# Kernel optimization log

Measured on AMD Instinct MI355X. Metric: run time of the kernel, lower is better.

The kernel has to match this reference:

```python
import jax, jax.numpy as jnp
import numpy as np

B, N, IN_DIM = 2, 512, 512
MEM, HID = 300, 64
NEG_SLOPE = 0.01


def setup_inputs() -> dict:
    key = jax.random.key(0)
    ks = jax.random.split(key, 10)
    feature = jax.random.normal(ks[0], (B, N, IN_DIM), dtype=jnp.float32)
    adj = jax.random.randint(ks[1], (B, N, N), 0, 2).astype(jnp.float32)
    s = 0.05
    # per-layer node projections W[l]
    w0 = jax.random.normal(ks[2], (IN_DIM, MEM), dtype=jnp.float32) * s
    b0 = jnp.zeros((MEM,), dtype=jnp.float32)
    w1 = jax.random.normal(ks[3], (MEM, MEM), dtype=jnp.float32) * s
    b1 = jnp.zeros((MEM,), dtype=jnp.float32)
    # shared attention MLP (afcs): Linear(2*MEM, HID) -> ReLU -> Linear(HID, 1)
    a1_w = jax.random.normal(ks[4], (2 * MEM, HID), dtype=jnp.float32) * s
    a1_b = jnp.zeros((HID,), dtype=jnp.float32)
    a2_w = jax.random.normal(ks[5], (HID, 1), dtype=jnp.float32) * s
    a2_b = jnp.zeros((1,), dtype=jnp.float32)
    return {"feature": feature, "adj": adj, "w0": w0, "b0": b0, "w1": w1,
            "b1": b1, "a1_w": a1_w, "a1_b": a1_b, "a2_w": a2_w, "a2_b": a2_b}


def _gat_layer(h_in, adj, w, b, a1_w, a1_b, a2_w, a2_b):
    h = h_in @ w + b                                   # (B,N,M)
    # cat([h_i, h_j]) @ a1_w split into the two halves (same math, no N^2*2M tensor)
    s_i = h @ a1_w[:MEM]                               # (B,N,H)
    s_j = h @ a1_w[MEM:]                               # (B,N,H)
    z = jax.nn.relu(s_i[:, :, None, :] + s_j[:, None, :, :] + a1_b)   # (B,N,N,H)
    e = (z @ a2_w)[..., 0] + a2_b[0]                   # (B,N,N)
    e = jax.nn.leaky_relu(e, negative_slope=NEG_SLOPE)
    b_, n_ = adj.shape[0], adj.shape[1]
    dmask = adj.reshape(b_, n_ * n_)
    logits = e.reshape(b_, n_ * n_) * dmask + (1.0 - dmask) * (-1e30)
    # NOTE: softmax over ALL N*N flattened edges (faithful to original dim=1)
    att = jax.nn.softmax(logits, axis=1).reshape(b_, n_, n_)
    return jnp.einsum('bij,bjd->bid', att, h)


def reference(feature, adj, w0, b0, w1, b1, a1_w, a1_b, a2_w, a2_b):
    f = _gat_layer(feature, adj, w0, b0, a1_w, a1_b, a2_w, a2_b)
    f = _gat_layer(f, adj, w1, b1, a1_w, a1_b, a2_w, a2_b)  # dropout = identity (eval)
    return f
```

## Files before the change

### kernel.cpp

```cpp
#include <hip/hip_runtime.h>

namespace {

constexpr int B_  = 2;
constexpr int N_  = 512;
constexpr int IN_ = 512;
constexpr int M_  = 300;
constexpr int H_  = 64;
constexpr float SLOPE_ = 0.01f;

constexpr long OFF_W0AI = 0;
constexpr long OFF_W0AJ = OFF_W0AI + 512L * 64;
constexpr long OFF_W1AI = OFF_W0AJ + 512L * 64;
constexpr long OFF_W1AJ = OFF_W1AI + 300L * 64;
constexpr long OFF_BSI0 = OFF_W1AJ + 300L * 64;
constexpr long OFF_BSJ0 = OFF_BSI0 + 64;
constexpr long OFF_BSI1 = OFF_BSJ0 + 64;
constexpr long OFF_BSJ1 = OFF_BSI1 + 64;
constexpr long OFF_H0   = OFF_BSJ1 + 64;
constexpr long OFF_SI0  = OFF_H0   + 1024L * 300;
constexpr long OFF_SJ0  = OFF_SI0  + 1024L * 64;
constexpr long OFF_F1   = OFF_SJ0  + 1024L * 64;
constexpr long OFF_H1   = OFF_F1   + 1024L * 300;
constexpr long OFF_SI1  = OFF_H1   + 1024L * 300;
constexpr long OFF_SJ1  = OFF_SI1  + 1024L * 64;
constexpr long OFF_ZP0  = OFF_SJ1  + 1024L * 64;
constexpr long OFF_ZP1  = OFF_ZP0  + 512;
constexpr long OFF_P0   = OFF_ZP1  + 512;
constexpr long OFF_P1   = OFF_P0   + 2L * 512 * 512;

struct Jobs {
    const float* A[8]; const float* W[8]; const float* bias[8]; const float* Zp[8];
    float* C[8];
    int K[8]; int lda[8]; int Cc[8]; int R[8];
    int off[8]; int njobs;
};

__global__ __launch_bounds__(256)
void gemm_multi(Jobs jb)
{
    __shared__ __align__(16) float As[32][38];
    __shared__ __align__(16) float Ws[32][64];

    const int bid = blockIdx.x;
    int j = jb.njobs - 1;
    while (j > 0 && bid < jb.off[j]) --j;
    const int local = bid - jb.off[j];

    const float* __restrict__ A = jb.A[j];
    const float* __restrict__ W = jb.W[j];
    const float* bias = jb.bias[j];
    const float* Zp   = jb.Zp[j];
    float* __restrict__ C = jb.C[j];
    const int K = jb.K[j], lda = jb.lda[j], Cc = jb.Cc[j], R = jb.R[j];

    const int tx   = (Cc + 63) >> 6;
    const int row0 = (local / tx) * 32;
    const int col0 = (local % tx) * 64;

    const int t   = threadIdx.x;
    const int ar  = t >> 3;
    const int ak  = (t & 7) * 4;
    const int arow = min(row0 + ar, R - 1);
    const int wk  = t >> 4;
    const int wc  = (t & 15) * 4;
    const int tm0 = (t >> 4) * 2;
    const int tn0 = (t & 15) * 4;

    auto loadA = [&](int k0) -> float4 {
        const int k = k0 + ak;
        if (k + 3 < K) return *(const float4*)(A + (long)arow * lda + k);
        float tv[4];
        #pragma unroll
        for (int u = 0; u < 4; ++u)
            tv[u] = (k + u < K) ? A[(long)arow * lda + k + u] : 0.0f;
        return make_float4(tv[0], tv[1], tv[2], tv[3]);
    };
    auto loadW = [&](int k0, int s) -> float4 {
        const int gk = k0 + wk + 16 * s;
        if (gk < K) {
            const int c = col0 + wc;
            if (c + 3 < Cc) return *(const float4*)(W + (long)gk * Cc + c);
            float tv[4];
            #pragma unroll
            for (int u = 0; u < 4; ++u)
                tv[u] = (c + u < Cc) ? W[(long)gk * Cc + c + u] : 0.0f;
            return make_float4(tv[0], tv[1], tv[2], tv[3]);
        }
        return make_float4(0.f, 0.f, 0.f, 0.f);
    };

    float acc[2][4] = {};
    float4 av  = loadA(0);
    float4 wv0 = loadW(0, 0);
    float4 wv1 = loadW(0, 1);

    for (int k0 = 0; k0 < K; k0 += 32) {
        As[ak + 0][ar] = av.x;
        As[ak + 1][ar] = av.y;
        As[ak + 2][ar] = av.z;
        As[ak + 3][ar] = av.w;
        *(float4*)&Ws[wk][wc]      = wv0;
        *(float4*)&Ws[wk + 16][wc] = wv1;
        __syncthreads();

        if (k0 + 32 < K) {
            av  = loadA(k0 + 32);
            wv0 = loadW(k0 + 32, 0);
            wv1 = loadW(k0 + 32, 1);
        }

        #pragma unroll
        for (int k = 0; k < 32; ++k) {
            const float a0 = As[k][tm0];
            const float a1 = As[k][tm0 + 1];
            const float4 w4 = *(const float4*)&Ws[k][tn0];
            acc[0][0] = fmaf(a0, w4.x, acc[0][0]);
            acc[0][1] = fmaf(a0, w4.y, acc[0][1]);
            acc[0][2] = fmaf(a0, w4.z, acc[0][2]);
            acc[0][3] = fmaf(a0, w4.w, acc[0][3]);
            acc[1][0] = fmaf(a1, w4.x, acc[1][0]);
            acc[1][1] = fmaf(a1, w4.y, acc[1][1]);
            acc[1][2] = fmaf(a1, w4.z, acc[1][2]);
            acc[1][3] = fmaf(a1, w4.w, acc[1][3]);
        }
        __syncthreads();
    }

    float scale = 1.0f;
    if (Zp != nullptr) {
        float s0 = 0.f, s1 = 0.f, s2 = 0.f, s3 = 0.f;
        for (int u = 0; u < 256; u += 4) {
            s0 += Zp[u]; s1 += Zp[u + 1]; s2 += Zp[u + 2]; s3 += Zp[u + 3];
        }
        scale = 1.0f / ((s0 + s1) + (s2 + s3));
    }
    const int cbase = col0 + tn0;
    float bv[4] = {0.f, 0.f, 0.f, 0.f};
    if (bias != nullptr) {
        #pragma unroll
        for (int u = 0; u < 4; ++u)
            if (cbase + u < Cc) bv[u] = bias[cbase + u];
    }
    #pragma unroll
    for (int i = 0; i < 2; ++i) {
        const int r = row0 + tm0 + i;
        if (r < R) {
            if (cbase + 3 < Cc) {
                float4 o;
                o.x = fmaf(acc[i][0], scale, bv[0]);
                o.y = fmaf(acc[i][1], scale, bv[1]);
                o.z = fmaf(acc[i][2], scale, bv[2]);
                o.w = fmaf(acc[i][3], scale, bv[3]);
                *(float4*)(C + (long)r * Cc + cbase) = o;
            } else {
                #pragma unroll
                for (int u = 0; u < 4; ++u)
                    if (cbase + u < Cc)
                        C[(long)r * Cc + cbase + u] = fmaf(acc[i][u], scale, bv[u]);
            }
        }
    }
}

__global__ __launch_bounds__(256)
void attn_p_kernel(const float* __restrict__ si, const float* __restrict__ sj,
                   const float* __restrict__ adj, const float* __restrict__ a2w,
                   const float* __restrict__ a2b, float* __restrict__ p,
                   float* __restrict__ Zpart)
{
    __shared__ __align__(16) float Si[32][68];
    __shared__ __align__(16) float Sj[32][68];

    const int b  = blockIdx.z;
    const int i0 = blockIdx.y * 32;
    const int j0 = blockIdx.x * 32;
    const int t  = threadIdx.x;

    {
        const int r  = t >> 3;
        const int hc = (t & 7) * 8;
        const float* gi = si + ((long)(b * N_ + i0 + r)) * H_ + hc;
        const float* gj = sj + ((long)(b * N_ + j0 + r)) * H_ + hc;
        *(float4*)&Si[r][hc]     = *(const float4*)(gi);
        *(float4*)&Si[r][hc + 4] = *(const float4*)(gi + 4);
        *(float4*)&Sj[r][hc]     = *(const float4*)(gj);
        *(float4*)&Sj[r][hc + 4] = *(const float4*)(gj + 4);
    }
    __syncthreads();

    const int i  = t >> 3;
    const int jl = t & 7;

    float e[4] = {0.f, 0.f, 0.f, 0.f};
    #pragma unroll
    for (int h0 = 0; h0 < H_; h0 += 4) {
        const float4 a4 = *(const float4*)&Si[i][h0];
        const float w0v = a2w[h0 + 0];
        const float w1v = a2w[h0 + 1];
        const float w2v = a2w[h0 + 2];
        const float w3v = a2w[h0 + 3];
        #pragma unroll
        for (int u = 0; u < 4; ++u) {
            const float4 b4 = *(const float4*)&Sj[jl + 8 * u][h0];
            e[u] = fmaf(fmaxf(a4.x + b4.x, 0.f), w0v, e[u]);
            e[u] = fmaf(fmaxf(a4.y + b4.y, 0.f), w1v, e[u]);
            e[u] = fmaf(fmaxf(a4.z + b4.z, 0.f), w2v, e[u]);
            e[u] = fmaf(fmaxf(a4.w + b4.w, 0.f), w3v, e[u]);
        }
    }

    const float a2bv = a2b[0];
    const long rowbase = ((long)(b * N_ + i0 + i)) * N_ + j0 + jl;
    float lsum = 0.f;
    #pragma unroll
    for (int u = 0; u < 4; ++u) {
        float ev = e[u] + a2bv;
        ev = (ev >= 0.f) ? ev : SLOPE_ * ev;
        const float m  = adj[rowbase + 8 * u];
        const float pv = m * __expf(ev);
        p[rowbase + 8 * u] = pv;
        lsum += pv;
    }

    #pragma unroll
    for (int off = 32; off > 0; off >>= 1)
        lsum += __shfl_down(lsum, off, 64);
    __shared__ float red[4];
    if ((t & 63) == 0) red[t >> 6] = lsum;
    __syncthreads();
    if (t == 0)
        Zpart[b * 256 + blockIdx.y * 16 + blockIdx.x] =
            red[0] + red[1] + red[2] + red[3];
}

}

extern "C" void kernel_launch(void* const* d_in, const int* in_sizes, int n_in,
                              void* d_out, int out_size, void* d_ws, size_t ws_size,
                              hipStream_t stream)
{
    const float* feature = (const float*)d_in[0];
    const float* adj     = (const float*)d_in[1];
    const float* w0      = (const float*)d_in[2];
    const float* b0      = (const float*)d_in[3];
    const float* w1      = (const float*)d_in[4];
    const float* b1      = (const float*)d_in[5];
    const float* a1w     = (const float*)d_in[6];
    const float* a1b     = (const float*)d_in[7];
    const float* a2w     = (const float*)d_in[8];
    const float* a2b     = (const float*)d_in[9];
    float* out = (float*)d_out;
    float* ws  = (float*)d_ws;

    float* cW0Ai = ws + OFF_W0AI;
    float* cW0Aj = ws + OFF_W0AJ;
    float* cW1Ai = ws + OFF_W1AI;
    float* cW1Aj = ws + OFF_W1AJ;
    float* bsi0  = ws + OFF_BSI0;
    float* bsj0  = ws + OFF_BSJ0;
    float* bsi1  = ws + OFF_BSI1;
    float* bsj1  = ws + OFF_BSJ1;
    float* h0    = ws + OFF_H0;
    float* si0   = ws + OFF_SI0;
    float* sj0   = ws + OFF_SJ0;
    float* f1    = ws + OFF_F1;
    float* h1    = ws + OFF_H1;
    float* si1   = ws + OFF_SI1;
    float* sj1   = ws + OFF_SJ1;
    float* Zp0   = ws + OFF_ZP0;
    float* Zp1   = ws + OFF_ZP1;
    float* p0    = ws + OFF_P0;
    float* p1    = ws + OFF_P1;

    const float* Ai = a1w;
    const float* Aj = a1w + (long)M_ * H_;

    auto set_job = [](Jobs& jb, int j, const float* A, const float* W,
                      const float* bias, const float* Zp, float* C,
                      int K, int lda, int Cc, int R, int& tiles) {
        jb.A[j] = A; jb.W[j] = W; jb.bias[j] = bias; jb.Zp[j] = Zp; jb.C[j] = C;
        jb.K[j] = K; jb.lda[j] = lda; jb.Cc[j] = Cc; jb.R[j] = R;
        jb.off[j] = tiles;
        tiles += ((R + 31) / 32) * ((Cc + 63) / 64);
    };

    {
        Jobs jb; int tiles = 0;
        set_job(jb, 0, w0, Ai, nullptr, nullptr, cW0Ai, M_, M_, H_, IN_, tiles);
        set_job(jb, 1, w0, Aj, nullptr, nullptr, cW0Aj, M_, M_, H_, IN_, tiles);
        set_job(jb, 2, w1, Ai, nullptr, nullptr, cW1Ai, M_, M_, H_, M_,  tiles);
        set_job(jb, 3, w1, Aj, nullptr, nullptr, cW1Aj, M_, M_, H_, M_,  tiles);
        set_job(jb, 4, b0, Ai, nullptr, nullptr, bsi0,  M_, M_, H_, 1,   tiles);
        set_job(jb, 5, b0, Aj, a1b,     nullptr, bsj0,  M_, M_, H_, 1,   tiles);
        set_job(jb, 6, b1, Ai, nullptr, nullptr, bsi1,  M_, M_, H_, 1,   tiles);
        set_job(jb, 7, b1, Aj, a1b,     nullptr, bsj1,  M_, M_, H_, 1,   tiles);
        jb.njobs = 8;
        gemm_multi<<<dim3(tiles), dim3(256), 0, stream>>>(jb);
    }

    {
        Jobs jb; int tiles = 0;
        set_job(jb, 0, feature, w0,    b0,   nullptr, h0,  IN_, IN_, M_, 1024, tiles);
        set_job(jb, 1, feature, cW0Ai, bsi0, nullptr, si0, IN_, IN_, H_, 1024, tiles);
        set_job(jb, 2, feature, cW0Aj, bsj0, nullptr, sj0, IN_, IN_, H_, 1024, tiles);
        jb.njobs = 3;
        gemm_multi<<<dim3(tiles), dim3(256), 0, stream>>>(jb);
    }

    attn_p_kernel<<<dim3(16, 16, B_), dim3(256), 0, stream>>>(
        si0, sj0, adj, a2w, a2b, p0, Zp0);

    {
        Jobs jb; int tiles = 0;
        set_job(jb, 0, p0,               h0,            nullptr, Zp0,       f1,
                N_, N_, M_, N_, tiles);
        set_job(jb, 1, p0 + (long)N_*N_, h0 + (long)N_*M_, nullptr, Zp0 + 256,
                f1 + (long)N_*M_, N_, N_, M_, N_, tiles);
        jb.njobs = 2;
        gemm_multi<<<dim3(tiles), dim3(256), 0, stream>>>(jb);
    }

    {
        Jobs jb; int tiles = 0;
        set_job(jb, 0, f1, w1,    b1,   nullptr, h1,  M_, M_, M_, 1024, tiles);
        set_job(jb, 1, f1, cW1Ai, bsi1, nullptr, si1, M_, M_, H_, 1024, tiles);
        set_job(jb, 2, f1, cW1Aj, bsj1, nullptr, sj1, M_, M_, H_, 1024, tiles);
        jb.njobs = 3;
        gemm_multi<<<dim3(tiles), dim3(256), 0, stream>>>(jb);
    }

    attn_p_kernel<<<dim3(16, 16, B_), dim3(256), 0, stream>>>(
        si1, sj1, adj, a2w, a2b, p1, Zp1);

    {
        Jobs jb; int tiles = 0;
        set_job(jb, 0, p1,               h1,            nullptr, Zp1,       out,
                N_, N_, M_, N_, tiles);
        set_job(jb, 1, p1 + (long)N_*N_, h1 + (long)N_*M_, nullptr, Zp1 + 256,
                out + (long)N_*M_, N_, N_, M_, N_, tiles);
        jb.njobs = 2;
        gemm_multi<<<dim3(tiles), dim3(256), 0, stream>>>(jb);
    }
}
```

Baseline: 173.4 us.

## Add split-K with atomic accumulation to batched GEMM launches

Splits the K dimension of every GEMM job into several slices, each run by its own block, and accumulates the partial tiles into zeroed outputs with float atomics. A new zero_ws kernel clears the intermediate buffers and the output beforehand. Bias is added only by slice 0, and the Zp normalizer sum becomes a wavefront shuffle reduction. The aim is more blocks to fill the many compute units on these small GEMMs, at the cost of atomic traffic, an extra launch and non-deterministic summation order.

```diff
diff --git a/kernel.cpp b/kernel.cpp
--- a/kernel.cpp
+++ b/kernel.cpp
@@ -29,18 +29,38 @@
 constexpr long OFF_P0   = OFF_ZP1  + 512;
 constexpr long OFF_P1   = OFF_P0   + 2L * 512 * 512;
 
+__device__ inline void atomAddF32(float* p, float v) {
+#if defined(__gfx90a__) || defined(__gfx940__) || defined(__gfx941__) || \
+    defined(__gfx942__) || defined(__gfx950__)
+    unsafeAtomicAdd(p, v);
+#else
+    atomicAdd(p, v);
+#endif
+}
+
+__global__ __launch_bounds__(256)
+void zero_ws(float4* __restrict__ a, int na4, float4* __restrict__ b, int nb4)
+{
+    const int i = blockIdx.x * 256 + threadIdx.x;
+    const int stride = gridDim.x * 256;
+    const float4 z = make_float4(0.f, 0.f, 0.f, 0.f);
+    for (int k = i; k < na4; k += stride) a[k] = z;
+    for (int k = i; k < nb4; k += stride) b[k] = z;
+}
+
 struct Jobs {
     const float* A[8]; const float* W[8]; const float* bias[8]; const float* Zp[8];
     float* C[8];
     int K[8]; int lda[8]; int Cc[8]; int R[8];
-    int off[8]; int njobs;
+    int off[8]; int split[8]; int njobs;
 };
 
-__global__ __launch_bounds__(256)
+__global__ __launch_bounds__(256, 4)
 void gemm_multi(Jobs jb)
 {
     __shared__ __align__(16) float As[32][38];
     __shared__ __align__(16) float Ws[32][64];
+    __shared__ float zred[4];
 
     const int bid = blockIdx.x;
     int j = jb.njobs - 1;
@@ -53,10 +73,20 @@
     const float* Zp   = jb.Zp[j];
     float* __restrict__ C = jb.C[j];
     const int K = jb.K[j], lda = jb.lda[j], Cc = jb.Cc[j], R = jb.R[j];
-
-    const int tx   = (Cc + 63) >> 6;
-    const int row0 = (local / tx) * 32;
-    const int col0 = (local % tx) * 64;
+    const int split = jb.split[j];
+
+    const int tx  = (Cc + 63) >> 6;
+    const int ty  = (R + 31) >> 5;
+    const int nrc = tx * ty;
+    const int tile  = local % nrc;
+    const int slice = local / nrc;
+    const int row0 = (tile / tx) * 32;
+    const int col0 = (tile % tx) * 64;
+
+    const int nslab = (K + 31) >> 5;
+    const int spl   = (nslab + split - 1) / split;
+    const int kb    = slice * spl * 32;
+    const int Ke    = min(K, kb + spl * 32);
 
     const int t   = threadIdx.x;
     const int ar  = t >> 3;
@@ -69,16 +99,16 @@
 
     auto loadA = [&](int k0) -> float4 {
         const int k = k0 + ak;
-        if (k + 3 < K) return *(const float4*)(A + (long)arow * lda + k);
+        if (k + 3 < Ke) return *(const float4*)(A + (long)arow * lda + k);
         float tv[4];
         #pragma unroll
         for (int u = 0; u < 4; ++u)
-            tv[u] = (k + u < K) ? A[(long)arow * lda + k + u] : 0.0f;
+            tv[u] = (k + u < Ke) ? A[(long)arow * lda + k + u] : 0.0f;
         return make_float4(tv[0], tv[1], tv[2], tv[3]);
     };
     auto loadW = [&](int k0, int s) -> float4 {
         const int gk = k0 + wk + 16 * s;
-        if (gk < K) {
+        if (gk < Ke) {
             const int c = col0 + wc;
             if (c + 3 < Cc) return *(const float4*)(W + (long)gk * Cc + c);
             float tv[4];
@@ -91,11 +121,11 @@
     };
 
     float acc[2][4] = {};
-    float4 av  = loadA(0);
-    float4 wv0 = loadW(0, 0);
-    float4 wv1 = loadW(0, 1);
-
-    for (int k0 = 0; k0 < K; k0 += 32) {
+    float4 av  = loadA(kb);
+    float4 wv0 = loadW(kb, 0);
+    float4 wv1 = loadW(kb, 1);
+
+    for (int k0 = kb; k0 < Ke; k0 += 32) {
         As[ak + 0][ar] = av.x;
         As[ak + 1][ar] = av.y;
         As[ak + 2][ar] = av.z;
@@ -104,7 +134,7 @@
         *(float4*)&Ws[wk + 16][wc] = wv1;
         __syncthreads();
 
-        if (k0 + 32 < K) {
+        if (k0 + 32 < Ke) {
             av  = loadA(k0 + 32);
             wv0 = loadW(k0 + 32, 0);
             wv1 = loadW(k0 + 32, 1);
@@ -129,15 +159,18 @@
 
     float scale = 1.0f;
     if (Zp != nullptr) {
-        float s0 = 0.f, s1 = 0.f, s2 = 0.f, s3 = 0.f;
-        for (int u = 0; u < 256; u += 4) {
-            s0 += Zp[u]; s1 += Zp[u + 1]; s2 += Zp[u + 2]; s3 += Zp[u + 3];
-        }
-        scale = 1.0f / ((s0 + s1) + (s2 + s3));
-    }
+        float v = Zp[t];
+        #pragma unroll
+        for (int off = 32; off > 0; off >>= 1)
+            v += __shfl_down(v, off, 64);
+        if ((t & 63) == 0) zred[t >> 6] = v;
+        __syncthreads();
+        scale = 1.0f / (zred[0] + zred[1] + zred[2] + zred[3]);
+    }
+
     const int cbase = col0 + tn0;
     float bv[4] = {0.f, 0.f, 0.f, 0.f};
-    if (bias != nullptr) {
+    if (bias != nullptr && slice == 0) {
         #pragma unroll
         for (int u = 0; u < 4; ++u)
             if (cbase + u < Cc) bv[u] = bias[cbase + u];
@@ -146,18 +179,27 @@
     for (int i = 0; i < 2; ++i) {
         const int r = row0 + tm0 + i;
         if (r < R) {
-            if (cbase + 3 < Cc) {
-                float4 o;
-                o.x = fmaf(acc[i][0], scale, bv[0]);
-                o.y = fmaf(acc[i][1], scale, bv[1]);
-                o.z = fmaf(acc[i][2], scale, bv[2]);
-                o.w = fmaf(acc[i][3], scale, bv[3]);
-                *(float4*)(C + (long)r * Cc + cbase) = o;
+            if (split == 1) {
+                if (cbase + 3 < Cc) {
+                    float4 o;
+                    o.x = fmaf(acc[i][0], scale, bv[0]);
+                    o.y = fmaf(acc[i][1], scale, bv[1]);
+                    o.z = fmaf(acc[i][2], scale, bv[2]);
+                    o.w = fmaf(acc[i][3], scale, bv[3]);
+                    *(float4*)(C + (long)r * Cc + cbase) = o;
+                } else {
+                    #pragma unroll
+                    for (int u = 0; u < 4; ++u)
+                        if (cbase + u < Cc)
+                            C[(long)r * Cc + cbase + u] =
+                                fmaf(acc[i][u], scale, bv[u]);
+                }
             } else {
                 #pragma unroll
                 for (int u = 0; u < 4; ++u)
                     if (cbase + u < Cc)
-                        C[(long)r * Cc + cbase + u] = fmaf(acc[i][u], scale, bv[u]);
+                        atomAddF32(C + (long)r * Cc + cbase + u,
+                                   fmaf(acc[i][u], scale, bv[u]));
             }
         }
     }
@@ -278,32 +320,37 @@
 
     auto set_job = [](Jobs& jb, int j, const float* A, const float* W,
                       const float* bias, const float* Zp, float* C,
-                      int K, int lda, int Cc, int R, int& tiles) {
+                      int K, int lda, int Cc, int R, int split, int& tiles) {
         jb.A[j] = A; jb.W[j] = W; jb.bias[j] = bias; jb.Zp[j] = Zp; jb.C[j] = C;
         jb.K[j] = K; jb.lda[j] = lda; jb.Cc[j] = Cc; jb.R[j] = R;
+        jb.split[j] = split;
         jb.off[j] = tiles;
-        tiles += ((R + 31) / 32) * ((Cc + 63) / 64);
+        tiles += ((R + 31) / 32) * ((Cc + 63) / 64) * split;
     };
 
-    {
-        Jobs jb; int tiles = 0;
-        set_job(jb, 0, w0, Ai, nullptr, nullptr, cW0Ai, M_, M_, H_, IN_, tiles);
-        set_job(jb, 1, w0, Aj, nullptr, nullptr, cW0Aj, M_, M_, H_, IN_, tiles);
-        set_job(jb, 2, w1, Ai, nullptr, nullptr, cW1Ai, M_, M_, H_, M_,  tiles);
-        set_job(jb, 3, w1, Aj, nullptr, nullptr, cW1Aj, M_, M_, H_, M_,  tiles);
-        set_job(jb, 4, b0, Ai, nullptr, nullptr, bsi0,  M_, M_, H_, 1,   tiles);
-        set_job(jb, 5, b0, Aj, a1b,     nullptr, bsj0,  M_, M_, H_, 1,   tiles);
-        set_job(jb, 6, b1, Ai, nullptr, nullptr, bsi1,  M_, M_, H_, 1,   tiles);
-        set_job(jb, 7, b1, Aj, a1b,     nullptr, bsj1,  M_, M_, H_, 1,   tiles);
+    zero_ws<<<dim3(1024), dim3(256), 0, stream>>>(
+        (float4*)ws, (int)(OFF_ZP0 / 4),
+        (float4*)out, (int)(2L * N_ * M_ / 4));
+
+    {
+        Jobs jb; int tiles = 0;
+        set_job(jb, 0, w0, Ai, nullptr, nullptr, cW0Ai, M_, M_, H_, IN_, 4, tiles);
+        set_job(jb, 1, w0, Aj, nullptr, nullptr, cW0Aj, M_, M_, H_, IN_, 4, tiles);
+        set_job(jb, 2, w1, Ai, nullptr, nullptr, cW1Ai, M_, M_, H_, M_,  4, tiles);
+        set_job(jb, 3, w1, Aj, nullptr, nullptr, cW1Aj, M_, M_, H_, M_,  4, tiles);
+        set_job(jb, 4, b0, Ai, nullptr, nullptr, bsi0,  M_, M_, H_, 1,   2, tiles);
+        set_job(jb, 5, b0, Aj, a1b,     nullptr, bsj0,  M_, M_, H_, 1,   2, tiles);
+        set_job(jb, 6, b1, Ai, nullptr, nullptr, bsi1,  M_, M_, H_, 1,   2, tiles);
+        set_job(jb, 7, b1, Aj, a1b,     nullptr, bsj1,  M_, M_, H_, 1,   2, tiles);
         jb.njobs = 8;
         gemm_multi<<<dim3(tiles), dim3(256), 0, stream>>>(jb);
     }
 
     {
         Jobs jb; int tiles = 0;
-        set_job(jb, 0, feature, w0,    b0,   nullptr, h0,  IN_, IN_, M_, 1024, tiles);
-        set_job(jb, 1, feature, cW0Ai, bsi0, nullptr, si0, IN_, IN_, H_, 1024, tiles);
-        set_job(jb, 2, feature, cW0Aj, bsj0, nullptr, sj0, IN_, IN_, H_, 1024, tiles);
+        set_job(jb, 0, feature, w0,    b0,   nullptr, h0,  IN_, IN_, M_, 1024, 4, tiles);
+        set_job(jb, 1, feature, cW0Ai, bsi0, nullptr, si0, IN_, IN_, H_, 1024, 4, tiles);
+        set_job(jb, 2, feature, cW0Aj, bsj0, nullptr, sj0, IN_, IN_, H_, 1024, 4, tiles);
         jb.njobs = 3;
         gemm_multi<<<dim3(tiles), dim3(256), 0, stream>>>(jb);
     }
@@ -313,19 +360,19 @@
 
     {
         Jobs jb; int tiles = 0;
-        set_job(jb, 0, p0,               h0,            nullptr, Zp0,       f1,
-                N_, N_, M_, N_, tiles);
+        set_job(jb, 0, p0,               h0,              nullptr, Zp0,       f1,
+                N_, N_, M_, N_, 6, tiles);
         set_job(jb, 1, p0 + (long)N_*N_, h0 + (long)N_*M_, nullptr, Zp0 + 256,
-                f1 + (long)N_*M_, N_, N_, M_, N_, tiles);
+                f1 + (long)N_*M_, N_, N_, M_, N_, 6, tiles);
         jb.njobs = 2;
         gemm_multi<<<dim3(tiles), dim3(256), 0, stream>>>(jb);
     }
 
     {
         Jobs jb; int tiles = 0;
-        set_job(jb, 0, f1, w1,    b1,   nullptr, h1,  M_, M_, M_, 1024, tiles);
-        set_job(jb, 1, f1, cW1Ai, bsi1, nullptr, si1, M_, M_, H_, 1024, tiles);
-        set_job(jb, 2, f1, cW1Aj, bsj1, nullptr, sj1, M_, M_, H_, 1024, tiles);
+        set_job(jb, 0, f1, w1,    b1,   nullptr, h1,  M_, M_, M_, 1024, 3, tiles);
+        set_job(jb, 1, f1, cW1Ai, bsi1, nullptr, si1, M_, M_, H_, 1024, 3, tiles);
+        set_job(jb, 2, f1, cW1Aj, bsj1, nullptr, sj1, M_, M_, H_, 1024, 3, tiles);
         jb.njobs = 3;
         gemm_multi<<<dim3(tiles), dim3(256), 0, stream>>>(jb);
     }
@@ -335,10 +382,10 @@
 
     {
         Jobs jb; int tiles = 0;
-        set_job(jb, 0, p1,               h1,            nullptr, Zp1,       out,
-                N_, N_, M_, N_, tiles);
+        set_job(jb, 0, p1,               h1,              nullptr, Zp1,       out,
+                N_, N_, M_, N_, 6, tiles);
         set_job(jb, 1, p1 + (long)N_*N_, h1 + (long)N_*M_, nullptr, Zp1 + 256,
-                out + (long)N_*M_, N_, N_, M_, N_, tiles);
+                out + (long)N_*M_, N_, N_, M_, N_, 6, tiles);
         jb.njobs = 2;
         gemm_multi<<<dim3(tiles), dim3(256), 0, stream>>>(jb);
     }
```

Measured after the change: 236.2 us. 1.36x slower.

## Fuse attention weights with P·H product via split-K partial slices

Applied to the files above, without the earlier changes.

Attention scoring is fused with the P·h matmul: each block computes a 32x64 tile of unnormalized exp weights in shared memory and multiplies it directly against the matching h rows. Each block writes one of eight split-K partial slices instead of materializing the full N×N P matrix. The next layer's GEMM sums the eight slices while loading A and applies the softmax normalization. A small finalize kernel does the same for the output. Layer-0 score projections now run after h0 is computed instead of through precomputed folded weights. This removes the P round-trip through memory and several launches, at the cost of 8x partial-slice traffic and an extra dependency step.

```diff
diff --git a/kernel.cpp b/kernel.cpp
--- a/kernel.cpp
+++ b/kernel.cpp
@@ -9,51 +9,32 @@
 constexpr int H_  = 64;
 constexpr float SLOPE_ = 0.01f;
 
-constexpr long OFF_W0AI = 0;
-constexpr long OFF_W0AJ = OFF_W0AI + 512L * 64;
-constexpr long OFF_W1AI = OFF_W0AJ + 512L * 64;
-constexpr long OFF_W1AJ = OFF_W1AI + 300L * 64;
-constexpr long OFF_BSI0 = OFF_W1AJ + 300L * 64;
-constexpr long OFF_BSJ0 = OFF_BSI0 + 64;
-constexpr long OFF_BSI1 = OFF_BSJ0 + 64;
-constexpr long OFF_BSJ1 = OFF_BSI1 + 64;
-constexpr long OFF_H0   = OFF_BSJ1 + 64;
-constexpr long OFF_SI0  = OFF_H0   + 1024L * 300;
-constexpr long OFF_SJ0  = OFF_SI0  + 1024L * 64;
-constexpr long OFF_F1   = OFF_SJ0  + 1024L * 64;
-constexpr long OFF_H1   = OFF_F1   + 1024L * 300;
-constexpr long OFF_SI1  = OFF_H1   + 1024L * 300;
-constexpr long OFF_SJ1  = OFF_SI1  + 1024L * 64;
-constexpr long OFF_ZP0  = OFF_SJ1  + 1024L * 64;
-constexpr long OFF_ZP1  = OFF_ZP0  + 512;
-constexpr long OFF_P0   = OFF_ZP1  + 512;
-constexpr long OFF_P1   = OFF_P0   + 2L * 512 * 512;
-
-struct Jobs {
-    const float* A[8]; const float* W[8]; const float* bias[8]; const float* Zp[8];
-    float* C[8];
-    int K[8]; int lda[8]; int Cc[8]; int R[8];
-    int off[8]; int njobs;
-};
-
-__global__ __launch_bounds__(256)
-void gemm_multi(Jobs jb)
+constexpr long OFF_CW1AI = 0;
+constexpr long OFF_CW1AJ = OFF_CW1AI + 300L * 64;
+constexpr long OFF_BSI1  = OFF_CW1AJ + 300L * 64;
+constexpr long OFF_BSJ1  = OFF_BSI1  + 64;
+constexpr long OFF_H0    = OFF_BSJ1  + 64;
+constexpr long OFF_SI0   = OFF_H0    + 307200;
+constexpr long OFF_SJ0   = OFF_SI0   + 65536;
+constexpr long OFF_H1    = OFF_SJ0   + 65536;
+constexpr long OFF_SI1   = OFF_H1    + 307200;
+constexpr long OFF_SJ1   = OFF_SI1   + 65536;
+constexpr long OFF_ZP0   = OFF_SJ1   + 65536;
+constexpr long OFF_ZP1   = OFF_ZP0   + 256;
+constexpr long OFF_SLC   = OFF_ZP1   + 256;
+
+__device__ __forceinline__ float4 f4add(float4 a, float4 b) {
+    a.x += b.x; a.y += b.y; a.z += b.z; a.w += b.w; return a;
+}
+
+template<int AFOLD>
+__device__ __forceinline__ void gemm_tile(
+    const float* __restrict__ A, long afstride,
+    const float* __restrict__ W, const float* __restrict__ bias,
+    const float* __restrict__ Zp, float* __restrict__ C,
+    int K, int lda, int Cc, int R, int local,
+    float (*As)[38], float (*Ws)[64], float* zred)
 {
-    __shared__ __align__(16) float As[32][38];
-    __shared__ __align__(16) float Ws[32][64];
-
-    const int bid = blockIdx.x;
-    int j = jb.njobs - 1;
-    while (j > 0 && bid < jb.off[j]) --j;
-    const int local = bid - jb.off[j];
-
-    const float* __restrict__ A = jb.A[j];
-    const float* __restrict__ W = jb.W[j];
-    const float* bias = jb.bias[j];
-    const float* Zp   = jb.Zp[j];
-    float* __restrict__ C = jb.C[j];
-    const int K = jb.K[j], lda = jb.lda[j], Cc = jb.Cc[j], R = jb.R[j];
-
     const int tx   = (Cc + 63) >> 6;
     const int row0 = (local / tx) * 32;
     const int col0 = (local % tx) * 64;
@@ -69,12 +50,24 @@
 
     auto loadA = [&](int k0) -> float4 {
         const int k = k0 + ak;
-        if (k + 3 < K) return *(const float4*)(A + (long)arow * lda + k);
-        float tv[4];
-        #pragma unroll
-        for (int u = 0; u < 4; ++u)
-            tv[u] = (k + u < K) ? A[(long)arow * lda + k + u] : 0.0f;
-        return make_float4(tv[0], tv[1], tv[2], tv[3]);
+        const long base = (long)arow * lda + k;
+        float4 r = make_float4(0.f, 0.f, 0.f, 0.f);
+        if (k + 3 < K) {
+            #pragma unroll
+            for (int s = 0; s < AFOLD; ++s)
+                r = f4add(r, *(const float4*)(A + (long)s * afstride + base));
+        } else {
+            #pragma unroll
+            for (int u = 0; u < 4; ++u)
+                if (k + u < K) {
+                    float v = 0.f;
+                    #pragma unroll
+                    for (int s = 0; s < AFOLD; ++s)
+                        v += A[(long)s * afstride + base + u];
+                    (&r.x)[u] = v;
+                }
+        }
+        return r;
     };
     auto loadW = [&](int k0, int s) -> float4 {
         const int gk = k0 + wk + 16 * s;
@@ -129,12 +122,16 @@
 
     float scale = 1.0f;
     if (Zp != nullptr) {
-        float s0 = 0.f, s1 = 0.f, s2 = 0.f, s3 = 0.f;
-        for (int u = 0; u < 256; u += 4) {
-            s0 += Zp[u]; s1 += Zp[u + 1]; s2 += Zp[u + 2]; s3 += Zp[u + 3];
-        }
-        scale = 1.0f / ((s0 + s1) + (s2 + s3));
-    }
+        const int zoff = (row0 >= 512) ? 128 : 0;
+        float v = (t < 128) ? Zp[zoff + t] : 0.f;
+        #pragma unroll
+        for (int off = 32; off > 0; off >>= 1)
+            v += __shfl_down(v, off, 64);
+        if ((t & 63) == 0) zred[t >> 6] = v;
+        __syncthreads();
+        scale = 1.0f / (zred[0] + zred[1] + zred[2] + zred[3]);
+    }
+
     const int cbase = col0 + tn0;
     float bv[4] = {0.f, 0.f, 0.f, 0.f};
     if (bias != nullptr) {
@@ -163,36 +160,75 @@
     }
 }
 
+struct JobsK {
+    const float* A[5]; long afstride[5];
+    const float* W[5]; const float* bias[5]; const float* Zp[5];
+    float* C[5];
+    int K[5]; int lda[5]; int Cc[5]; int R[5];
+    int off[5]; int njobs;
+};
+
+template<int AFOLD>
 __global__ __launch_bounds__(256)
-void attn_p_kernel(const float* __restrict__ si, const float* __restrict__ sj,
-                   const float* __restrict__ adj, const float* __restrict__ a2w,
-                   const float* __restrict__ a2b, float* __restrict__ p,
-                   float* __restrict__ Zpart)
+void gemm_jobs(JobsK jb)
+{
+    __shared__ __align__(16) float As[32][38];
+    __shared__ __align__(16) float Ws[32][64];
+    __shared__ float zred[4];
+
+    const int bid = blockIdx.x;
+    int j = jb.njobs - 1;
+    while (j > 0 && bid < jb.off[j]) --j;
+    const int local = bid - jb.off[j];
+
+    gemm_tile<AFOLD>(jb.A[j], jb.afstride[j], jb.W[j], jb.bias[j], jb.Zp[j],
+                     jb.C[j], jb.K[j], jb.lda[j], jb.Cc[j], jb.R[j],
+                     local, As, Ws, zred);
+}
+
+__global__ __launch_bounds__(256)
+void attn_pv(const float* __restrict__ si, const float* __restrict__ sj,
+             const float* __restrict__ adj, const float* __restrict__ a2w,
+             const float* __restrict__ a2b, const float* __restrict__ h,
+             float* __restrict__ slc, float* __restrict__ Zpart)
 {
     __shared__ __align__(16) float Si[32][68];
-    __shared__ __align__(16) float Sj[32][68];
-
-    const int b  = blockIdx.z;
-    const int i0 = blockIdx.y * 32;
-    const int j0 = blockIdx.x * 32;
-    const int t  = threadIdx.x;
+    __shared__ __align__(16) float Sj[64][68];
+    __shared__ __align__(16) float Pt[64][36];
+    __shared__ __align__(16) float Hs[64][68];
+    __shared__ float red[4];
+
+    const int bid = blockIdx.x;
+    const int b   = bid >> 7;
+    const int rr_ = bid & 127;
+    const int it  = rr_ >> 3;
+    const int js  = rr_ & 7;
+    const int i0  = it * 32;
+    const int j0  = js * 64;
+    const int t   = threadIdx.x;
 
     {
         const int r  = t >> 3;
         const int hc = (t & 7) * 8;
         const float* gi = si + ((long)(b * N_ + i0 + r)) * H_ + hc;
-        const float* gj = sj + ((long)(b * N_ + j0 + r)) * H_ + hc;
         *(float4*)&Si[r][hc]     = *(const float4*)(gi);
         *(float4*)&Si[r][hc + 4] = *(const float4*)(gi + 4);
-        *(float4*)&Sj[r][hc]     = *(const float4*)(gj);
-        *(float4*)&Sj[r][hc + 4] = *(const float4*)(gj + 4);
+    }
+    {
+        const int r  = t >> 2;
+        const int hc = (t & 3) * 16;
+        const float* gj = sj + ((long)(b * N_ + j0 + r)) * H_ + hc;
+        *(float4*)&Sj[r][hc]      = *(const float4*)(gj);
+        *(float4*)&Sj[r][hc + 4]  = *(const float4*)(gj + 4);
+        *(float4*)&Sj[r][hc + 8]  = *(const float4*)(gj + 8);
+        *(float4*)&Sj[r][hc + 12] = *(const float4*)(gj + 12);
     }
     __syncthreads();
 
     const int i  = t >> 3;
     const int jl = t & 7;
 
-    float e[4] = {0.f, 0.f, 0.f, 0.f};
+    float e[8] = {0.f, 0.f, 0.f, 0.f, 0.f, 0.f, 0.f, 0.f};
     #pragma unroll
     for (int h0 = 0; h0 < H_; h0 += 4) {
         const float4 a4 = *(const float4*)&Si[i][h0];
@@ -201,7 +237,7 @@
         const float w2v = a2w[h0 + 2];
         const float w3v = a2w[h0 + 3];
         #pragma unroll
-        for (int u = 0; u < 4; ++u) {
+        for (int u = 0; u < 8; ++u) {
             const float4 b4 = *(const float4*)&Sj[jl + 8 * u][h0];
             e[u] = fmaf(fmaxf(a4.x + b4.x, 0.f), w0v, e[u]);
             e[u] = fmaf(fmaxf(a4.y + b4.y, 0.f), w1v, e[u]);
@@ -214,24 +250,103 @@
     const long rowbase = ((long)(b * N_ + i0 + i)) * N_ + j0 + jl;
     float lsum = 0.f;
     #pragma unroll
-    for (int u = 0; u < 4; ++u) {
+    for (int u = 0; u < 8; ++u) {
         float ev = e[u] + a2bv;
         ev = (ev >= 0.f) ? ev : SLOPE_ * ev;
         const float m  = adj[rowbase + 8 * u];
         const float pv = m * __expf(ev);
-        p[rowbase + 8 * u] = pv;
+        Pt[jl + 8 * u][i] = pv;
         lsum += pv;
     }
 
     #pragma unroll
     for (int off = 32; off > 0; off >>= 1)
         lsum += __shfl_down(lsum, off, 64);
-    __shared__ float red[4];
     if ((t & 63) == 0) red[t >> 6] = lsum;
     __syncthreads();
     if (t == 0)
-        Zpart[b * 256 + blockIdx.y * 16 + blockIdx.x] =
-            red[0] + red[1] + red[2] + red[3];
+        Zpart[b * 128 + it * 8 + js] = red[0] + red[1] + red[2] + red[3];
+
+    const int tm0 = (t >> 4) * 2;
+    const int tn0 = (t & 15) * 4;
+    float* dst = slc + (long)js * 307200;
+
+    for (int cc = 0; cc < 5; ++cc) {
+        const int c0 = cc * 64;
+        {
+            const int r  = t >> 2;
+            const int hc = (t & 3) * 16;
+            const float* gh = h + ((long)(b * N_ + j0 + r)) * M_ + c0 + hc;
+            if (c0 + hc + 15 < M_) {
+                *(float4*)&Hs[r][hc]      = *(const float4*)(gh);
+                *(float4*)&Hs[r][hc + 4]  = *(const float4*)(gh + 4);
+                *(float4*)&Hs[r][hc + 8]  = *(const float4*)(gh + 8);
+                *(float4*)&Hs[r][hc + 12] = *(const float4*)(gh + 12);
+            } else {
+                #pragma unroll
+                for (int u = 0; u < 16; ++u)
+                    Hs[r][hc + u] = (c0 + hc + u < M_) ? gh[u] : 0.f;
+            }
+        }
+        __syncthreads();
+
+        float acc[2][4] = {};
+        #pragma unroll
+        for (int k = 0; k < 64; ++k) {
+            const float a0 = Pt[k][tm0];
+            const float a1 = Pt[k][tm0 + 1];
+            const float4 w4 = *(const float4*)&Hs[k][tn0];
+            acc[0][0] = fmaf(a0, w4.x, acc[0][0]);
+            acc[0][1] = fmaf(a0, w4.y, acc[0][1]);
+            acc[0][2] = fmaf(a0, w4.z, acc[0][2]);
+            acc[0][3] = fmaf(a0, w4.w, acc[0][3]);
+            acc[1][0] = fmaf(a1, w4.x, acc[1][0]);
+            acc[1][1] = fmaf(a1, w4.y, acc[1][1]);
+            acc[1][2] = fmaf(a1, w4.z, acc[1][2]);
+            acc[1][3] = fmaf(a1, w4.w, acc[1][3]);
+        }
+
+        const int cb = c0 + tn0;
+        #pragma unroll
+        for (int ii = 0; ii < 2; ++ii) {
+            const long r = (long)(b * N_ + i0 + tm0 + ii);
+            if (cb + 3 < M_) {
+                *(float4*)(dst + r * M_ + cb) =
+                    make_float4(acc[ii][0], acc[ii][1], acc[ii][2], acc[ii][3]);
+            } else {
+                #pragma unroll
+                for (int u = 0; u < 4; ++u)
+                    if (cb + u < M_) dst[r * M_ + cb + u] = acc[ii][u];
+            }
+        }
+        __syncthreads();
+    }
+}
+
+__global__ __launch_bounds__(256)
+void finalize(const float* __restrict__ slc, const float* __restrict__ Zp,
+              float* __restrict__ out)
+{
+    __shared__ float red[4];
+    const int t = threadIdx.x;
+
+    float v = Zp[t];
+    #pragma unroll
+    for (int off = 32; off > 0; off >>= 1)
+        v += __shfl_down(v, off, 64);
+    if ((t & 63) == 0) red[t >> 6] = v;
+    __syncthreads();
+    const float s0 = 1.0f / (red[0] + red[1]);
+    const float s1 = 1.0f / (red[2] + red[3]);
+
+    const int idx = blockIdx.x * 256 + t;
+    const float4* src = (const float4*)slc;
+    float4 a = src[idx];
+    #pragma unroll
+    for (int s = 1; s < 8; ++s) a = f4add(a, src[idx + s * 76800]);
+    const float sc = (idx < 38400) ? s0 : s1;
+    a.x *= sc; a.y *= sc; a.z *= sc; a.w *= sc;
+    ((float4*)out)[idx] = a;
 }
 
 }
@@ -240,6 +355,7 @@
                               void* d_out, int out_size, void* d_ws, size_t ws_size,
                               hipStream_t stream)
 {
+    (void)in_sizes; (void)n_in; (void)out_size; (void)ws_size;
     const float* feature = (const float*)d_in[0];
     const float* adj     = (const float*)d_in[1];
     const float* w0      = (const float*)d_in[2];
@@ -253,93 +369,66 @@
     float* out = (float*)d_out;
     float* ws  = (float*)d_ws;
 
-    float* cW0Ai = ws + OFF_W0AI;
-    float* cW0Aj = ws + OFF_W0AJ;
-    float* cW1Ai = ws + OFF_W1AI;
-    float* cW1Aj = ws + OFF_W1AJ;
-    float* bsi0  = ws + OFF_BSI0;
-    float* bsj0  = ws + OFF_BSJ0;
+    float* cW1Ai = ws + OFF_CW1AI;
+    float* cW1Aj = ws + OFF_CW1AJ;
     float* bsi1  = ws + OFF_BSI1;
     float* bsj1  = ws + OFF_BSJ1;
     float* h0    = ws + OFF_H0;
     float* si0   = ws + OFF_SI0;
     float* sj0   = ws + OFF_SJ0;
-    float* f1    = ws + OFF_F1;
     float* h1    = ws + OFF_H1;
     float* si1   = ws + OFF_SI1;
     float* sj1   = ws + OFF_SJ1;
     float* Zp0   = ws + OFF_ZP0;
     float* Zp1   = ws + OFF_ZP1;
-    float* p0    = ws + OFF_P0;
-    float* p1    = ws + OFF_P1;
+    float* slc   = ws + OFF_SLC;
 
     const float* Ai = a1w;
     const float* Aj = a1w + (long)M_ * H_;
 
-    auto set_job = [](Jobs& jb, int j, const float* A, const float* W,
-                      const float* bias, const float* Zp, float* C,
-                      int K, int lda, int Cc, int R, int& tiles) {
-        jb.A[j] = A; jb.W[j] = W; jb.bias[j] = bias; jb.Zp[j] = Zp; jb.C[j] = C;
+    auto set_job = [](JobsK& jb, int j, const float* A, long afstride,
+                      const float* W, const float* bias, const float* Zp,
+                      float* C, int K, int lda, int Cc, int R, int& tiles) {
+        jb.A[j] = A; jb.afstride[j] = afstride;
+        jb.W[j] = W; jb.bias[j] = bias; jb.Zp[j] = Zp; jb.C[j] = C;
         jb.K[j] = K; jb.lda[j] = lda; jb.Cc[j] = Cc; jb.R[j] = R;
         jb.off[j] = tiles;
         tiles += ((R + 31) / 32) * ((Cc + 63) / 64);
     };
 
     {
-        Jobs jb; int tiles = 0;
-        set_job(jb, 0, w0, Ai, nullptr, nullptr, cW0Ai, M_, M_, H_, IN_, tiles);
-        set_job(jb, 1, w0, Aj, nullptr, nullptr, cW0Aj, M_, M_, H_, IN_, tiles);
-        set_job(jb, 2, w1, Ai, nullptr, nullptr, cW1Ai, M_, M_, H_, M_,  tiles);
-        set_job(jb, 3, w1, Aj, nullptr, nullptr, cW1Aj, M_, M_, H_, M_,  tiles);
-        set_job(jb, 4, b0, Ai, nullptr, nullptr, bsi0,  M_, M_, H_, 1,   tiles);
-        set_job(jb, 5, b0, Aj, a1b,     nullptr, bsj0,  M_, M_, H_, 1,   tiles);
-        set_job(jb, 6, b1, Ai, nullptr, nullptr, bsi1,  M_, M_, H_, 1,   tiles);
-        set_job(jb, 7, b1, Aj, a1b,     nullptr, bsj1,  M_, M_, H_, 1,   tiles);
-        jb.njobs = 8;
-        gemm_multi<<<dim3(tiles), dim3(256), 0, stream>>>(jb);
+        JobsK jb; int tiles = 0;
+        set_job(jb, 0, feature, 0, w0, b0,   nullptr, h0,    IN_, IN_, M_, 1024, tiles);
+        set_job(jb, 1, w1,      0, Ai, nullptr, nullptr, cW1Ai, M_, M_, H_, M_, tiles);
+        set_job(jb, 2, w1,      0, Aj, nullptr, nullptr, cW1Aj, M_, M_, H_, M_, tiles);
+        set_job(jb, 3, b1,      0, Ai, nullptr, nullptr, bsi1,  M_, M_, H_, 1,  tiles);
+        set_job(jb, 4, b1,      0, Aj, a1b,     nullptr, bsj1,  M_, M_, H_, 1,  tiles);
+        jb.njobs = 5;
+        gemm_jobs<1><<<dim3(tiles), dim3(256), 0, stream>>>(jb);
     }
 
     {
-        Jobs jb; int tiles = 0;
-        set_job(jb, 0, feature, w0,    b0,   nullptr, h0,  IN_, IN_, M_, 1024, tiles);
-        set_job(jb, 1, feature, cW0Ai, bsi0, nullptr, si0, IN_, IN_, H_, 1024, tiles);
-        set_job(jb, 2, feature, cW0Aj, bsj0, nullptr, sj0, IN_, IN_, H_, 1024, tiles);
+        JobsK jb; int tiles = 0;
+        set_job(jb, 0, h0, 0, Ai, nullptr, nullptr, si0, M_, M_, H_, 1024, tiles);
+        set_job(jb, 1, h0, 0, Aj, a1b,     nullptr, sj0, M_, M_, H_, 1024, tiles);
+        jb.njobs = 2;
+        gemm_jobs<1><<<dim3(tiles), dim3(256), 0, stream>>>(jb);
+    }
+
+    attn_pv<<<dim3(256), dim3(256), 0, stream>>>(
+        si0, sj0, adj, a2w, a2b, h0, slc, Zp0);
+
+    {
+        JobsK jb; int tiles = 0;
+        set_job(jb, 0, slc, 307200, w1,    b1,   Zp0, h1,  M_, M_, M_, 1024, tiles);
+        set_job(jb, 1, slc, 307200, cW1Ai, bsi1, Zp0, si1, M_, M_, H_, 1024, tiles);
+        set_job(jb, 2, slc, 307200, cW1Aj, bsj1, Zp0, sj1, M_, M_, H_, 1024, tiles);
         jb.njobs = 3;
-        gemm_multi<<<dim3(tiles), dim3(256), 0, stream>>>(jb);
-    }
-
-    attn_p_kernel<<<dim3(16, 16, B_), dim3(256), 0, stream>>>(
-        si0, sj0, adj, a2w, a2b, p0, Zp0);
-
-    {
-        Jobs jb; int tiles = 0;
-        set_job(jb, 0, p0,               h0,            nullptr, Zp0,       f1,
-                N_, N_, M_, N_, tiles);
-        set_job(jb, 1, p0 + (long)N_*N_, h0 + (long)N_*M_, nullptr, Zp0 + 256,
-                f1 + (long)N_*M_, N_, N_, M_, N_, tiles);
-        jb.njobs = 2;
-        gemm_multi<<<dim3(tiles), dim3(256), 0, stream>>>(jb);
-    }
-
-    {
-        Jobs jb; int tiles = 0;
-        set_job(jb, 0, f1, w1,    b1,   nullptr, h1,  M_, M_, M_, 1024, tiles);
-        set_job(jb, 1, f1, cW1Ai, bsi1, nullptr, si1, M_, M_, H_, 1024, tiles);
-        set_job(jb, 2, f1, cW1Aj, bsj1, nullptr, sj1, M_, M_, H_, 1024, tiles);
-        jb.njobs = 3;
-        gemm_multi<<<dim3(tiles), dim3(256), 0, stream>>>(jb);
-    }
-
-    attn_p_kernel<<<dim3(16, 16, B_), dim3(256), 0, stream>>>(
-        si1, sj1, adj, a2w, a2b, p1, Zp1);
-
-    {
-        Jobs jb; int tiles = 0;
-        set_job(jb, 0, p1,               h1,            nullptr, Zp1,       out,
-                N_, N_, M_, N_, tiles);
-        set_job(jb, 1, p1 + (long)N_*N_, h1 + (long)N_*M_, nullptr, Zp1 + 256,
-                out + (long)N_*M_, N_, N_, M_, N_, tiles);
-        jb.njobs = 2;
-        gemm_multi<<<dim3(tiles), dim3(256), 0, stream>>>(jb);
-    }
-}
+        gemm_jobs<8><<<dim3(tiles), dim3(256), 0, stream>>>(jb);
+    }
+
+    attn_pv<<<dim3(256), dim3(256), 0, stream>>>(
+        si1, sj1, adj, a2w, a2b, h1, slc, Zp1);
+
+    finalize<<<dim3(300), dim3(256), 0, stream>>>(slc, Zp1, out);
+}
```

Result: slower. 182.8 us (+5.4%).
